# Kernel tuning notes

Hardware: AMD Instinct MI355X
Metric: run time of the kernel (lower is better)

## Reference

```python
import jax, jax.numpy as jnp
import numpy as np

B, S, HOPS, DIM, NREL = 1024, 32, 2, 64, 237
NENT, NEDGE = 14541, 272115
SIGMA = 0.1
CFMW = 64


def setup_inputs() -> dict:
    key = jax.random.key(0)
    ks = jax.random.split(key, 20)

    def g(k, shape):
        return (jax.random.normal(k, shape, dtype=jnp.float32) / np.float32(np.sqrt(shape[0])))

    inp = {
        "entity_pairs": jax.random.randint(ks[0], (B, 2), 0, NENT),
        "train_edges": jax.random.randint(ks[1], (B,), 0, NEDGE),
        "labels": jax.random.randint(ks[2], (B,), 0, NREL),
        "entity2edges": jax.random.randint(ks[3], (NENT + 1, S), 0, NEDGE + 1),
        "edge2entities": jax.random.randint(ks[4], (NEDGE + 1, 1), 0, NENT + 1),
        "edge2relation": jax.random.randint(ks[5], (NEDGE + 1,), 0, NREL + 1),
        "t": jax.random.uniform(ks[6], (B,), dtype=jnp.float32),
        "eps": jax.random.normal(ks[7], (B, NREL), dtype=jnp.float32),
        "rel_feat": g(ks[8], (NREL, DIM)),
        "W_agg0": g(ks[9], (DIM, DIM)), "b_agg0": jnp.zeros((DIM,), jnp.float32),
        "W_agg1": g(ks[10], (DIM, NREL)), "b_agg1": jnp.zeros((NREL,), jnp.float32),
        "W_out": g(ks[11], (2 * NREL, NREL)), "b_out": jnp.zeros((NREL,), jnp.float32),
        "mW1": g(ks[12], (NREL + 1, CFMW)), "mb1": jnp.zeros((CFMW,), jnp.float32),
        "mW2": g(ks[13], (CFMW, CFMW)), "mb2": jnp.zeros((CFMW,), jnp.float32),
        "mW3": g(ks[14], (CFMW, CFMW)), "mb3": jnp.zeros((CFMW,), jnp.float32),
        "mW4": g(ks[15], (CFMW, NREL)), "mb4": jnp.zeros((NREL,), jnp.float32),
    }
    return inp


def _side(ent, labels, train_edges, entity2edges, edge2entities, edge2relation, relf, aggs):
    # multi-hop neighbor edge gather + masks (exclude the training edge itself)
    edges_list = [labels]  # hop-0 "edges" are the relation labels
    masks = []
    for i in range(HOPS):
        if i == 0:
            ne = ent.reshape(B, 1)  # (B, 1) source entities
        else:
            ne = edge2entities[edges_list[-1].reshape(-1)].reshape(B, -1)
        nedges = entity2edges[ne.reshape(-1)].reshape(B, -1)  # (B, S**(i+1))
        edges_list.append(nedges)
        masks.append((nedges != train_edges[:, None]).astype(relf.dtype))
    # edge -> relation -> feature
    ev = [relf[edges_list[0]]]  # (B, DIM)
    for edges in edges_list[1:]:
        ev.append(relf[edge2relation[edges]])  # (B, S**h, DIM)
    # iterative mean aggregation (PathCon-style, one entity per edge)
    for i in range(HOPS):
        W, b, act, self_inc = aggs[i]
        d = W.shape[0]
        nxt = []
        for hop in range(HOPS - i):
            neigh = ev[hop + 1].reshape(B, -1, 1, S, d)
            m = masks[hop].reshape(B, -1, 1, S, 1)
            out = jnp.mean(jnp.mean(neigh * m, axis=-2), axis=-2)  # (B, S**hop, d)
            if self_inc:
                out = out + ev[hop].reshape(B, -1, d)
            nxt.append(act(out @ W + b))
        ev = nxt
    return ev[0].reshape(B, NREL)


def reference(entity_pairs, train_edges, labels, entity2edges, edge2entities,
              edge2relation, t, eps, rel_feat, W_agg0, b_agg0, W_agg1, b_agg1,
              W_out, b_out, mW1, mb1, mW2, mb2, mW3, mb3, mW4, mb4):
    relf = jnp.concatenate([rel_feat, jnp.zeros((1, DIM), rel_feat.dtype)], axis=0)
    aggs = [
        (W_agg0, b_agg0, jax.nn.relu, True),    # intermediate hop: relu, self-included
        (W_agg1, b_agg1, lambda x: x, False),   # last hop: identity, no self
    ]
    x0 = _side(entity_pairs[:, 0], labels, train_edges, entity2edges,
               edge2entities, edge2relation, relf, aggs)
    x1 = _side(entity_pairs[:, 1], labels, train_edges, entity2edges,
               edge2entities, edge2relation, relf, aggs)
    output = jnp.concatenate([x0, x1], axis=-1) @ W_out + b_out  # (B, NREL)
    # CFM: xt = (1-t) x0 + t x1 + sigma*eps ; ut = x1 - x0
    tb = t[:, None]
    xt = (1.0 - tb) * x0 + tb * x1 + SIGMA * eps
    h = jnp.concatenate([xt, tb], axis=-1)
    h = jax.nn.selu(h @ mW1 + mb1)
    h = jax.nn.selu(h @ mW2 + mb2)
    h = jax.nn.selu(h @ mW3 + mb3)
    vt = h @ mW4 + mb4
    scores = output * vt
    return scores
```

## Files before the change

### kernel.cpp

```cpp
#include <hip/hip_runtime.h>
#include <math.h>

#define BB 1024
#define S 32
#define DIM 64
#define NREL 237
#define SIGMA 0.1f

#define OFS_WC0   7616
#define N_WC      (64*237)
#define OFS_WC1   (OFS_WC0 + N_WC)
#define OFS_BC    (OFS_WC1 + N_WC)
#define OFS_HC    (OFS_BC + 237)

#define LDS_BYTES 44544

__device__ __forceinline__ float selu_f(float x) {
    const float alpha = 1.6732632423543772f;
    const float scale = 1.0507009873554805f;
    return scale * (x > 0.f ? x : alpha * expm1f(x));
}

__device__ __forceinline__ unsigned short f2bf(float f) {
    unsigned int b = __float_as_uint(f);
    return (unsigned short)((b + 0x7fffu + ((b >> 16) & 1u)) >> 16);
}

__global__ __launch_bounds__(256) void precompute_kernel(
    const float* __restrict__ rel_feat, const float* __restrict__ W0,
    const float* __restrict__ W1, const float* __restrict__ b1,
    const float* __restrict__ W_out, const float* __restrict__ b_out,
    const float* __restrict__ mW1, const float* __restrict__ mb1,
    float* __restrict__ ws) {
    __shared__ float red[256];
    int blk = blockIdx.x;
    const int tid = threadIdx.x;

    if (blk < 60) {
        int idx = blk * 256 + tid;
        if (idx < 238 * 64) {
            int r = idx >> 6, o = idx & 63;
            float acc = 0.f;
            if (r < NREL) {
#pragma unroll 8
                for (int d = 0; d < 64; ++d)
                    acc += rel_feat[r * 64 + d] * W0[d * 64 + o];
            }
            ((unsigned short*)ws)[idx] = f2bf(acc);
        }
        return;
    }
    blk -= 60;
    if (blk < 512) {
        int half = blk >> 8;
        int lb = blk & 255;
        int o = lb >> 2, ct = lb & 3;
        int cl = tid & 63, g = tid >> 6;
        int c = ct * 64 + cl;
        const float* Wsrc = W_out + half * 237 * 237;
        float acc = 0.f;
        if (c < NREL) {
            int k0 = g * 60, k1 = (g == 3) ? 237 : (k0 + 60);
#pragma unroll 4
            for (int k = k0; k < k1; ++k)
                acc += W1[o * 237 + k] * Wsrc[k * 237 + c];
        }
        red[tid] = acc;
        __syncthreads();
        if (g == 0 && c < NREL) {
            float s = red[cl] + red[64 + cl] + red[128 + cl] + red[192 + cl];
            ws[(half ? OFS_WC1 : OFS_WC0) + o * 237 + c] = s;
        }
        return;
    }
    blk -= 512;
    if (blk < 4) {
        int cl = tid & 63, g = tid >> 6;
        int c = blk * 64 + cl;
        float acc = 0.f;
        if (c < NREL) {
            int k0 = g * 60, k1 = (g == 3) ? 237 : (k0 + 60);
#pragma unroll 4
            for (int k = k0; k < k1; ++k)
                acc += b1[k] * (W_out[k * 237 + c] + W_out[(237 + k) * 237 + c]);
        }
        red[tid] = acc;
        __syncthreads();
        if (g == 0 && c < NREL)
            ws[OFS_BC + c] = b_out[c] + red[cl] + red[64 + cl] + red[128 + cl] + red[192 + cl];
        return;
    }
    {
        int w = tid & 63, g = tid >> 6;
        int k0 = g * 60, k1 = (g == 3) ? 237 : (k0 + 60);
        float acc = 0.f;
#pragma unroll 4
        for (int k = k0; k < k1; ++k)
            acc += b1[k] * mW1[k * 64 + w];
        red[tid] = acc;
        __syncthreads();
        if (g == 0)
            ws[OFS_HC + w] = mb1[w] + red[w] + red[64 + w] + red[128 + w] + red[192 + w];
    }
}

#define BF_ACC(sum, d) {                                                  \
    sum.x += __uint_as_float((d).x << 16);                                \
    sum.y += __uint_as_float((d).x & 0xffff0000u);                        \
    sum.z += __uint_as_float((d).y << 16);                                \
    sum.w += __uint_as_float((d).y & 0xffff0000u); }

__global__ __launch_bounds__(512) void gf_kernel(
    const int* __restrict__ ep, const int* __restrict__ te_arr,
    const int* __restrict__ e2e_tab, const int* __restrict__ e2ent,
    const int* __restrict__ e2r, const float* __restrict__ b0,
    const float* __restrict__ t_arr, const float* __restrict__ eps,
    const float* __restrict__ W1, const float* __restrict__ mW1,
    const float* __restrict__ mW2, const float* __restrict__ mb2,
    const float* __restrict__ mW3, const float* __restrict__ mb3,
    const float* __restrict__ mW4, const float* __restrict__ mb4,
    const float* __restrict__ ws, float* __restrict__ out) {
    extern __shared__ float smem[];
    unsigned short* s_wr = (unsigned short*)smem;
    int*   s_r2m  = (int*)(smem + 7616);
    int*   s_r1   = (int*)(smem + 8640);
    int*   s_ent2 = (int*)(smem + 8704);
    float* s_m1   = smem + 8768;
    float* s_v1   = smem + 8832;
    float* s_ov   = smem + 11008;

    const int tid = threadIdx.x;
    const int b = blockIdx.x;
    const int c = tid & 15;
    const int te = te_arr[b];
    const float4 b0v = ((const float4*)b0)[c];

    {
        const uint4* src = (const uint4*)ws;
        uint4* dst = (uint4*)s_wr;
        for (int i = tid; i < 1904; i += 512) dst[i] = src[i];
    }
    const uint2* W2 = (const uint2*)s_wr;

    if (tid < 64) {
        int u = tid >> 5, s = tid & 31;
        int ent = ep[b * 2 + u];
        int e1 = e2e_tab[ent * S + s];
        s_r1[u * 32 + s] = e2r[e1];
        s_m1[u * 32 + s] = (e1 != te) ? 1.0f : 0.0f;
        s_ent2[u * 32 + s] = e2ent[e1];
    }
    __syncthreads();

    for (int p = tid; p < 1024; p += 512) {
        int j = p >> 5, s = p & 31;
        int e2 = e2e_tab[s_ent2[j] * S + s];
        s_r2m[p] = (e2 == te) ? NREL : e2r[e2];
    }
    __syncthreads();

    const float inv = 1.0f / 32.0f;
    for (int u = 0; u < 2; ++u) {
        {
            const int j = tid >> 4;
            const int* rr = &s_r2m[j * 32];
            uint2 ds = W2[s_r1[u * 32 + j] * 16 + c];
            float4 self = make_float4(0.f, 0.f, 0.f, 0.f);
            BF_ACC(self, ds)
            float4 sa = make_float4(0.f, 0.f, 0.f, 0.f);
            float4 sb = make_float4(0.f, 0.f, 0.f, 0.f);
#pragma unroll
            for (int s = 0; s < 16; ++s) {
                uint2 d = W2[rr[s] * 16 + c];
                BF_ACC(sa, d)
            }
#pragma unroll
            for (int s = 16; s < 32; ++s) {
                uint2 d = W2[rr[s] * 16 + c];
                BF_ACC(sb, d)
            }
            float m = s_m1[u * 32 + j];
            float4 r;
            r.x = fmaxf(self.x + (sa.x + sb.x) * inv + b0v.x, 0.f) * m;
            r.y = fmaxf(self.y + (sa.y + sb.y) * inv + b0v.y, 0.f) * m;
            r.z = fmaxf(self.z + (sa.z + sb.z) * inv + b0v.z, 0.f) * m;
            r.w = fmaxf(self.w + (sa.w + sb.w) * inv + b0v.w, 0.f) * m;
            *((float4*)&s_v1[j * 68 + c * 4]) = r;
        }
        __syncthreads();
        if (tid < 64) {
            float sum = 0.f;
#pragma unroll 8
            for (int j = 0; j < 32; ++j) sum += s_v1[j * 68 + tid];
            s_ov[u * 64 + tid] = sum * inv;
        }
        if (u == 0) {
            for (int p = tid; p < 1024; p += 512) {
                int j = p >> 5, s = p & 31;
                int e2 = e2e_tab[s_ent2[32 + j] * S + s];
                s_r2m[p] = (e2 == te) ? NREL : e2r[e2];
            }
        }
        __syncthreads();
    }

    float* s_ymix = smem;
    float* s_outv = smem + 240;
    float* s_red  = smem + 480;
    float* s_h    = smem + 992;
    float* s_omix = smem + 1056;
    float* s_vp   = smem + 1120;
    const float tb = t_arr[b];
    const float* Wc0 = ws + OFS_WC0;
    const float* Wc1 = ws + OFS_WC1;
    const float* bc = ws + OFS_BC;
    const float* hc = ws + OFS_HC;

    if (tid < 64)
        s_omix[tid] = (1.f - tb) * s_ov[tid] + tb * s_ov[64 + tid];
    __syncthreads();

    if (tid < 256) {
        if (tid < NREL) {
            float y = 0.f;
#pragma unroll 4
            for (int d = 0; d < 64; ++d)
                y += s_omix[d] * W1[d * 237 + tid];
            s_ymix[tid] = y;
        }
    } else {
        int cc = tid - 256;
        if (cc < NREL) {
            float a = bc[cc];
#pragma unroll 4
            for (int d = 0; d < 64; ++d)
                a += s_ov[d] * Wc0[d * 237 + cc] + s_ov[64 + d] * Wc1[d * 237 + cc];
            s_outv[cc] = a;
        }
    }
    __syncthreads();

    {
        int w = tid & 63, q = tid >> 6;
        int k0 = q * 30, k1 = (q == 7) ? 237 : (k0 + 30);
        const float* e = eps + b * 237;
        float a = 0.f;
#pragma unroll 4
        for (int k = k0; k < k1; ++k)
            a += (SIGMA * e[k] + s_ymix[k]) * mW1[k * 64 + w];
        s_red[tid] = a;
    }
    __syncthreads();
    if (tid < 64) {
        float h = hc[tid] + tb * mW1[237 * 64 + tid];
#pragma unroll
        for (int q = 0; q < 8; ++q) h += s_red[q * 64 + tid];
        s_h[tid] = selu_f(h);
    }
    __syncthreads();

    {
        int w = tid & 63, q = tid >> 6;
        float a = 0.f;
#pragma unroll
        for (int d = q * 8; d < q * 8 + 8; ++d)
            a += s_h[d] * mW2[d * 64 + w];
        s_red[tid] = a;
    }
    __syncthreads();
    if (tid < 64) {
        float v = mb2[tid];
#pragma unroll
        for (int q = 0; q < 8; ++q) v += s_red[q * 64 + tid];
        s_h[tid] = selu_f(v);
    }
    __syncthreads();

    {
        int w = tid & 63, q = tid >> 6;
        float a = 0.f;
#pragma unroll
        for (int d = q * 8; d < q * 8 + 8; ++d)
            a += s_h[d] * mW3[d * 64 + w];
        s_red[tid] = a;
    }
    __syncthreads();
    if (tid < 64) {
        float v = mb3[tid];
#pragma unroll
        for (int q = 0; q < 8; ++q) v += s_red[q * 64 + tid];
        s_h[tid] = selu_f(v);
    }
    __syncthreads();

    {
        int half = tid >> 8, cc = tid & 255;
        if (cc < NREL) {
            float a = 0.f;
#pragma unroll 4
            for (int w = half * 32; w < half * 32 + 32; ++w)
                a += s_h[w] * mW4[w * 237 + cc];
            s_vp[half * 240 + cc] = a;
        }
    }
    __syncthreads();
    if (tid < NREL)
        out[b * 237 + tid] = s_outv[tid] * (mb4[tid] + s_vp[tid] + s_vp[240 + tid]);
}

extern "C" void kernel_launch(void* const* d_in, const int* in_sizes, int n_in,
                              void* d_out, int out_size, void* d_ws, size_t ws_size,
                              hipStream_t stream) {
    const int* ep       = (const int*)d_in[0];
    const int* te       = (const int*)d_in[1];
    const int* e2e      = (const int*)d_in[3];
    const int* e2ent    = (const int*)d_in[4];
    const int* e2r      = (const int*)d_in[5];
    const float* t      = (const float*)d_in[6];
    const float* eps    = (const float*)d_in[7];
    const float* relf   = (const float*)d_in[8];
    const float* W0     = (const float*)d_in[9];
    const float* b0     = (const float*)d_in[10];
    const float* W1     = (const float*)d_in[11];
    const float* b1     = (const float*)d_in[12];
    const float* W_out  = (const float*)d_in[13];
    const float* b_out  = (const float*)d_in[14];
    const float* mW1    = (const float*)d_in[15];
    const float* mb1    = (const float*)d_in[16];
    const float* mW2    = (const float*)d_in[17];
    const float* mb2    = (const float*)d_in[18];
    const float* mW3    = (const float*)d_in[19];
    const float* mb3    = (const float*)d_in[20];
    const float* mW4    = (const float*)d_in[21];
    const float* mb4    = (const float*)d_in[22];
    float* ws  = (float*)d_ws;
    float* out = (float*)d_out;

    hipLaunchKernelGGL(precompute_kernel, dim3(577), dim3(256), 0, stream,
                       relf, W0, W1, b1, W_out, b_out, mW1, mb1, ws);
    hipLaunchKernelGGL(gf_kernel, dim3(BB), dim3(512), LDS_BYTES, stream,
                       ep, te, e2e, e2ent, e2r, b0,
                       t, eps, W1, mW1, mW2, mb2, mW3, mb3, mW4, mb4, ws, out);
}
```

Before: 151.2 us.

## Precompute per-entity neighbor relation sums and correct for masked training edge

Adds an agg_kernel that, for every entity, sums the projected relation features of its 32 neighbor edges into a workspace table. The main kernel then reads that per-entity sum and subtracts the contribution of neighbor edges equal to the training edge, counted with wave shuffles, instead of gathering 32 rows per neighbor entity per sample. Relation projections are now stored in fp32 rather than bf16, LDS usage drops, and occupancy is hinted with launch bounds. The cost is an extra kernel that runs over all ~14.5k entities, plus the assumption that masked edges always map to the zero feature row.

```diff
diff --git a/kernel.cpp b/kernel.cpp
--- a/kernel.cpp
+++ b/kernel.cpp
@@ -5,25 +5,24 @@
 #define S 32
 #define DIM 64
 #define NREL 237
+#define NENT 14541
 #define SIGMA 0.1f
 
-#define OFS_WC0   7616
+#define OFS_WR    0
+#define N_WR      (238*64)
+#define OFS_WC0   15232
 #define N_WC      (64*237)
 #define OFS_WC1   (OFS_WC0 + N_WC)
 #define OFS_BC    (OFS_WC1 + N_WC)
 #define OFS_HC    (OFS_BC + 237)
-
-#define LDS_BYTES 44544
+#define OFS_A     45872
+
+#define LDS_BYTES 18688
 
 __device__ __forceinline__ float selu_f(float x) {
     const float alpha = 1.6732632423543772f;
     const float scale = 1.0507009873554805f;
     return scale * (x > 0.f ? x : alpha * expm1f(x));
-}
-
-__device__ __forceinline__ unsigned short f2bf(float f) {
-    unsigned int b = __float_as_uint(f);
-    return (unsigned short)((b + 0x7fffu + ((b >> 16) & 1u)) >> 16);
 }
 
 __global__ __launch_bounds__(256) void precompute_kernel(
@@ -46,7 +45,7 @@
                 for (int d = 0; d < 64; ++d)
                     acc += rel_feat[r * 64 + d] * W0[d * 64 + o];
             }
-            ((unsigned short*)ws)[idx] = f2bf(acc);
+            ws[OFS_WR + idx] = acc;
         }
         return;
     }
@@ -104,13 +103,35 @@
     }
 }
 
-#define BF_ACC(sum, d) {                                                  \
-    sum.x += __uint_as_float((d).x << 16);                                \
-    sum.y += __uint_as_float((d).x & 0xffff0000u);                        \
-    sum.z += __uint_as_float((d).y << 16);                                \
-    sum.w += __uint_as_float((d).y & 0xffff0000u); }
-
-__global__ __launch_bounds__(512) void gf_kernel(
+__global__ __launch_bounds__(256) void agg_kernel(
+    const int* __restrict__ e2e_tab, const int* __restrict__ e2r,
+    float* __restrict__ ws) {
+    __shared__ int s_r[512];
+    const int tid = threadIdx.x;
+    const int grp = tid >> 4, c = tid & 15;
+    const int ent = blockIdx.x * 16 + grp;
+    const bool ok = ent < (NENT + 1);
+    if (ok) {
+        int ea = e2e_tab[ent * S + c];
+        int eb = e2e_tab[ent * S + 16 + c];
+        s_r[grp * 32 + c] = e2r[ea];
+        s_r[grp * 32 + 16 + c] = e2r[eb];
+    }
+    __syncthreads();
+    if (ok) {
+        const float4* Wr4 = (const float4*)(ws + OFS_WR);
+        const int* rr = &s_r[grp * 32];
+        float4 acc = make_float4(0.f, 0.f, 0.f, 0.f);
+#pragma unroll
+        for (int s = 0; s < 32; ++s) {
+            float4 v = Wr4[rr[s] * 16 + c];
+            acc.x += v.x; acc.y += v.y; acc.z += v.z; acc.w += v.w;
+        }
+        ((float4*)(ws + OFS_A))[ent * 16 + c] = acc;
+    }
+}
+
+__global__ __launch_bounds__(512, 8) void gf_kernel(
     const int* __restrict__ ep, const int* __restrict__ te_arr,
     const int* __restrict__ e2e_tab, const int* __restrict__ e2ent,
     const int* __restrict__ e2r, const float* __restrict__ b0,
@@ -121,26 +142,22 @@
     const float* __restrict__ mW4, const float* __restrict__ mb4,
     const float* __restrict__ ws, float* __restrict__ out) {
     extern __shared__ float smem[];
-    unsigned short* s_wr = (unsigned short*)smem;
-    int*   s_r2m  = (int*)(smem + 7616);
-    int*   s_r1   = (int*)(smem + 8640);
-    int*   s_ent2 = (int*)(smem + 8704);
-    float* s_m1   = smem + 8768;
-    float* s_v1   = smem + 8832;
-    float* s_ov   = smem + 11008;
+    float* s_v1   = smem;
+    int*   s_r1   = (int*)(smem + 4352);
+    int*   s_ent2 = (int*)(smem + 4416);
+    float* s_m1   = smem + 4480;
+    float* s_ov   = smem + 4544;
 
     const int tid = threadIdx.x;
     const int b = blockIdx.x;
+    const int grp = tid >> 4;
     const int c = tid & 15;
     const int te = te_arr[b];
-    const float4 b0v = ((const float4*)b0)[c];
-
-    {
-        const uint4* src = (const uint4*)ws;
-        uint4* dst = (uint4*)s_wr;
-        for (int i = tid; i < 1904; i += 512) dst[i] = src[i];
-    }
-    const uint2* W2 = (const uint2*)s_wr;
+    const int rte = e2r[te];
+    const float4* Wr4 = (const float4*)(ws + OFS_WR);
+    const float4* A4  = (const float4*)(ws + OFS_A);
+    const float4 b0v  = ((const float4*)b0)[c];
+    const float4 wrte = Wr4[rte * 16 + c];
 
     if (tid < 64) {
         int u = tid >> 5, s = tid & 31;
@@ -152,57 +169,38 @@
     }
     __syncthreads();
 
-    for (int p = tid; p < 1024; p += 512) {
-        int j = p >> 5, s = p & 31;
-        int e2 = e2e_tab[s_ent2[j] * S + s];
-        s_r2m[p] = (e2 == te) ? NREL : e2r[e2];
-    }
-    __syncthreads();
-
     const float inv = 1.0f / 32.0f;
+#pragma unroll
     for (int u = 0; u < 2; ++u) {
-        {
-            const int j = tid >> 4;
-            const int* rr = &s_r2m[j * 32];
-            uint2 ds = W2[s_r1[u * 32 + j] * 16 + c];
-            float4 self = make_float4(0.f, 0.f, 0.f, 0.f);
-            BF_ACC(self, ds)
-            float4 sa = make_float4(0.f, 0.f, 0.f, 0.f);
-            float4 sb = make_float4(0.f, 0.f, 0.f, 0.f);
-#pragma unroll
-            for (int s = 0; s < 16; ++s) {
-                uint2 d = W2[rr[s] * 16 + c];
-                BF_ACC(sa, d)
-            }
-#pragma unroll
-            for (int s = 16; s < 32; ++s) {
-                uint2 d = W2[rr[s] * 16 + c];
-                BF_ACC(sb, d)
-            }
-            float m = s_m1[u * 32 + j];
-            float4 r;
-            r.x = fmaxf(self.x + (sa.x + sb.x) * inv + b0v.x, 0.f) * m;
-            r.y = fmaxf(self.y + (sa.y + sb.y) * inv + b0v.y, 0.f) * m;
-            r.z = fmaxf(self.z + (sa.z + sb.z) * inv + b0v.z, 0.f) * m;
-            r.w = fmaxf(self.w + (sa.w + sb.w) * inv + b0v.w, 0.f) * m;
-            *((float4*)&s_v1[j * 68 + c * 4]) = r;
-        }
-        __syncthreads();
-        if (tid < 64) {
-            float sum = 0.f;
+        const int j = grp;
+        const int ent2 = s_ent2[u * 32 + j];
+        int e2a = e2e_tab[ent2 * S + c];
+        int e2b = e2e_tab[ent2 * S + 16 + c];
+        int cnt = (e2a == te) + (e2b == te);
+        cnt += __shfl_xor(cnt, 1);
+        cnt += __shfl_xor(cnt, 2);
+        cnt += __shfl_xor(cnt, 4);
+        cnt += __shfl_xor(cnt, 8);
+        float4 a4   = A4[ent2 * 16 + c];
+        float4 self = Wr4[s_r1[u * 32 + j] * 16 + c];
+        float fc = (float)cnt;
+        float m = s_m1[u * 32 + j];
+        float4 r;
+        r.x = fmaxf(self.x + (a4.x - fc * wrte.x) * inv + b0v.x, 0.f) * m;
+        r.y = fmaxf(self.y + (a4.y - fc * wrte.y) * inv + b0v.y, 0.f) * m;
+        r.z = fmaxf(self.z + (a4.z - fc * wrte.z) * inv + b0v.z, 0.f) * m;
+        r.w = fmaxf(self.w + (a4.w - fc * wrte.w) * inv + b0v.w, 0.f) * m;
+        *((float4*)&s_v1[(u * 32 + j) * 68 + c * 4]) = r;
+    }
+    __syncthreads();
+    if (tid < 128) {
+        int u = tid >> 6, w = tid & 63;
+        float sum = 0.f;
 #pragma unroll 8
-            for (int j = 0; j < 32; ++j) sum += s_v1[j * 68 + tid];
-            s_ov[u * 64 + tid] = sum * inv;
-        }
-        if (u == 0) {
-            for (int p = tid; p < 1024; p += 512) {
-                int j = p >> 5, s = p & 31;
-                int e2 = e2e_tab[s_ent2[32 + j] * S + s];
-                s_r2m[p] = (e2 == te) ? NREL : e2r[e2];
-            }
-        }
-        __syncthreads();
-    }
+        for (int j = 0; j < 32; ++j) sum += s_v1[(u * 32 + j) * 68 + w];
+        s_ov[u * 64 + w] = sum * inv;
+    }
+    __syncthreads();
 
     float* s_ymix = smem;
     float* s_outv = smem + 240;
@@ -338,6 +336,8 @@
 
     hipLaunchKernelGGL(precompute_kernel, dim3(577), dim3(256), 0, stream,
                        relf, W0, W1, b1, W_out, b_out, mW1, mb1, ws);
+    hipLaunchKernelGGL(agg_kernel, dim3((NENT + 1 + 15) / 16), dim3(256), 0, stream,
+                       e2e, e2r, ws);
     hipLaunchKernelGGL(gf_kernel, dim3(BB), dim3(512), LDS_BYTES, stream,
                        ep, te, e2e, e2ent, e2r, b0,
                        t, eps, W1, mW1, mW2, mb2, mW3, mb3, mW4, mb4, ws, out);
```

Measured after the change: 142.1 us. 6.0% less time.
